# Performance work log

Hardware: AMD Instinct MI355X
Metric: run time of the kernel (lower is better)

## Reference

```python
import jax, jax.numpy as jnp
import numpy as np

B, C, K, H, W = 8, 64, 32, 128, 128  # K = num_cluster // 2
NEG_SLOPE = 0.1


def setup_inputs() -> dict:
    key = jax.random.key(0)
    k1, k2, k3, k4, k5, k6 = jax.random.split(key, 6)
    HR = jax.random.normal(k1, (B, C, H, W), jnp.float32)
    LR = jax.random.normal(k2, (B, C, H, W), jnp.float32)
    # Conv2d(1+K, 1, 1) weights flattened to [1+K] + bias, Conv2d(1,1,1) -> scalar w/b
    w1 = jax.random.normal(k3, (K + 1,), jnp.float32) * 0.1
    b1 = jax.random.normal(k4, (1,), jnp.float32) * 0.1
    w2 = jax.random.normal(k5, (1,), jnp.float32) * 0.1
    b2 = jax.random.normal(k6, (1,), jnp.float32) * 0.1
    return {"HR": HR, "LR": LR, "w1": w1, "b1": b1, "w2": w2, "b2": b2}


def reference(HR, LR, w1, b1, w2, b2):
    Bn, Cn = HR.shape[0], HR.shape[1]
    HRf = HR.reshape(Bn, Cn, -1)                      # [B, C, HW]
    LRf = LR.reshape(Bn, Cn, -1)                      # [B, C, HW]
    corr = jnp.einsum('bcn,bdn->bcd', LRf, HRf)       # [B, C_lr, C_hr]
    _, idx = jax.lax.top_k(corr, K)                   # [B, C, K] (int32)
    # gather top-K HR channels per LR channel: [B, C, K, H, W]
    gathered = jax.vmap(lambda h, ix: h[ix])(HR, idx)
    weight = jax.nn.sigmoid(jnp.max(gathered, axis=2))        # [B, C, H, W]
    # 1x1 conv over the (1+K) concatenated channels == weighted sum
    fusion = w1[0] * LR + jnp.einsum('bckhw,k->bchw', gathered, w1[1:]) + b1[0]
    fusion = jnp.where(fusion >= 0, fusion, NEG_SLOPE * fusion)  # LeakyReLU(0.1)
    fusion = w2[0] * fusion + b2[0]                   # second 1x1 conv
    return fusion * (1.0 + weight)                    # fusion + weight*fusion
```

## Files before the change

### kernel.cpp

```cpp
#include <hip/hip_runtime.h>
#include <math.h>

#define B_ 8
#define C_ 64
#define K_ 32
#define HW_ 16384
#define NCHUNKOUT_ 64
#define TILE_ 256
#define NEG_SLOPE_ 0.1f


__device__ __forceinline__ void gl_lds16(const float* g, float* l) {
    __builtin_amdgcn_global_load_lds(
        (const __attribute__((address_space(1))) void*)g,
        (__attribute__((address_space(3))) void*)l,
        16, 0, 0);
}

__global__ __launch_bounds__(256, 2) void corr_partial_kernel(
    const float* __restrict__ LR, const float* __restrict__ HR,
    float* __restrict__ partial)
{
    __shared__ float smem[16384];
    float* lrS = smem;
    float* hrS = smem + 8192;

    const int bid = blockIdx.x;
    const int b = bid >> 6;
    const int q = bid & 63;
    const int t = threadIdx.x;
    const int wv = t >> 6;
    const int lane = t & 63;
    const int cq = lane >> 3;
    const int dq = lane & 7;

    float acc[8][8] = {};

    #pragma unroll 1
    for (int it = 0; it < 2; ++it) {
        const int n0 = q * 256 + it * 128;
        if (it) __syncthreads();

        #pragma unroll
        for (int s = 0; s < 8; ++s) {
            const int r0 = wv * 16 + s * 2;
            const int row = r0 + (lane >> 5);
            const int cl = (((lane & 31) * 4) ^ ((row & 7) * 4));
            const size_t goff = (size_t)(b * C_ + row) * HW_ + n0 + cl;
            gl_lds16(&LR[goff], &lrS[r0 * 128]);
            gl_lds16(&HR[goff], &hrS[r0 * 128]);
        }
        __syncthreads();

        #pragma unroll
        for (int nq = 0; nq < 8; ++nq) {
            const int col = wv * 32 + nq * 4;
            const int cxl = col ^ (cq * 4);
            const int cxh = col ^ (dq * 4);
            float4 lv[8];
            #pragma unroll
            for (int i = 0; i < 8; ++i)
                lv[i] = *reinterpret_cast<const float4*>(&lrS[(cq + 8 * i) * 128 + cxl]);
            #pragma unroll
            for (int j = 0; j < 8; ++j) {
                const float4 hv = *reinterpret_cast<const float4*>(&hrS[(dq + 8 * j) * 128 + cxh]);
                #pragma unroll
                for (int i = 0; i < 8; ++i) {
                    acc[i][j] = fmaf(lv[i].x, hv.x, acc[i][j]);
                    acc[i][j] = fmaf(lv[i].y, hv.y, acc[i][j]);
                    acc[i][j] = fmaf(lv[i].z, hv.z, acc[i][j]);
                    acc[i][j] = fmaf(lv[i].w, hv.w, acc[i][j]);
                }
            }
        }
    }

    __syncthreads();
    float* red = smem;
    #pragma unroll
    for (int sl = 0; sl < 16; ++sl) {
        const int i = sl >> 1;
        const int j0 = (sl & 1) * 4;
        *reinterpret_cast<float4*>(&red[((wv * 16 + sl) * 64 + lane) * 4]) =
            make_float4(acc[i][j0], acc[i][j0 + 1], acc[i][j0 + 2], acc[i][j0 + 3]);
    }
    __syncthreads();

    float* P = partial + (size_t)bid * (C_ * C_);
    #pragma unroll
    for (int pp = 0; pp < 4; ++pp) {
        const int sl = wv * 4 + pp;
        float4 s = make_float4(0.f, 0.f, 0.f, 0.f);
        #pragma unroll
        for (int w = 0; w < 4; ++w) {
            const float4 v = *reinterpret_cast<const float4*>(
                &red[((w * 16 + sl) * 64 + lane) * 4]);
            s.x += v.x; s.y += v.y; s.z += v.z; s.w += v.w;
        }
        const int i = sl >> 1;
        const int j0 = (sl & 1) * 4;
        const int row = (lane >> 3) + 8 * i;
        const int colb = (lane & 7) + 8 * j0;
        P[row * C_ + colb]      = s.x;
        P[row * C_ + colb + 8]  = s.y;
        P[row * C_ + colb + 16] = s.z;
        P[row * C_ + colb + 24] = s.w;
    }
}

__global__ __launch_bounds__(64) void rank_kernel(
    const float* __restrict__ partial, int* __restrict__ idxb)
{
    __shared__ double vals[C_];
    const int blk = blockIdx.x;
    const int b = blk >> 6;
    const int c = blk & 63;
    const int d = threadIdx.x;

    double acc = 0.0;
    for (int k = 0; k < NCHUNKOUT_; ++k)
        acc += (double)partial[(size_t)(b * NCHUNKOUT_ + k) * (C_ * C_) + c * C_ + d];
    vals[d] = acc;
    __syncthreads();

    int r = 0;
    for (int jj = 0; jj < C_; ++jj) {
        const double vj = vals[jj];
        r += (int)((vj > acc) || (vj == acc && jj < d));
    }
    if (r < K_) idxb[blk * K_ + r] = d;
}

__global__ __launch_bounds__(512, 2) void fusion_gather_kernel(
    const float* __restrict__ HR, const float* __restrict__ LR,
    const int* __restrict__ idxb,
    const float* __restrict__ w1, const float* __restrict__ b1,
    const float* __restrict__ w2, const float* __restrict__ b2,
    float* __restrict__ out)
{
    __shared__ float hrS[C_][TILE_];

    const int t = threadIdx.x;
    const int bid = blockIdx.x;
    const int b = bid >> 6;
    const int px0 = (bid & 63) * TILE_;

    const float* HRb = HR + (size_t)b * C_ * HW_;
    #pragma unroll
    for (int i = 0; i < 8; ++i) {
        const int f = i * 512 + t;
        const int c = f >> 6;
        const int qq = f & 63;
        *reinterpret_cast<float4*>(&hrS[c][qq * 4]) =
            *reinterpret_cast<const float4*>(&HRb[(size_t)c * HW_ + px0 + qq * 4]);
    }
    __syncthreads();

    const int wv = t >> 6;
    const int lane = t & 63;
    const int p4 = lane * 4;

    const int* idxc = idxb + b * C_ * K_;
    const float w10 = w1[0];
    const float b1v = b1[0], w2v = w2[0], b2v = b2[0];

    #pragma unroll 1
    for (int ci = 0; ci < 8; ++ci) {
        const int c = wv * 8 + ci;
        const float4 l4 = *reinterpret_cast<const float4*>(
            &LR[(size_t)(b * C_ + c) * HW_ + px0 + p4]);
        float acc[4] = {0.f, 0.f, 0.f, 0.f};
        float mx[4]  = {-1e30f, -1e30f, -1e30f, -1e30f};
        #pragma unroll
        for (int k = 0; k < K_; ++k) {
            const int d = idxc[c * K_ + k];
            const float4 h = *reinterpret_cast<const float4*>(&hrS[d][p4]);
            const float wk = w1[k + 1];
            acc[0] = fmaf(h.x, wk, acc[0]);
            acc[1] = fmaf(h.y, wk, acc[1]);
            acc[2] = fmaf(h.z, wk, acc[2]);
            acc[3] = fmaf(h.w, wk, acc[3]);
            mx[0] = fmaxf(mx[0], h.x);
            mx[1] = fmaxf(mx[1], h.y);
            mx[2] = fmaxf(mx[2], h.z);
            mx[3] = fmaxf(mx[3], h.w);
        }
        const float l[4] = {l4.x, l4.y, l4.z, l4.w};
        float o[4];
        #pragma unroll
        for (int p = 0; p < 4; ++p) {
            float f = fmaf(w10, l[p], acc[p]) + b1v;
            f = f >= 0.f ? f : NEG_SLOPE_ * f;
            f = fmaf(w2v, f, b2v);
            const float s = 1.f / (1.f + __expf(-mx[p]));
            o[p] = f * (1.f + s);
        }
        *reinterpret_cast<float4*>(&out[(size_t)(b * C_ + c) * HW_ + px0 + p4]) =
            make_float4(o[0], o[1], o[2], o[3]);
    }
}

extern "C" void kernel_launch(void* const* d_in, const int* in_sizes, int n_in,
                              void* d_out, int out_size, void* d_ws, size_t ws_size,
                              hipStream_t stream)
{
    const float* HR = (const float*)d_in[0];
    const float* LR = (const float*)d_in[1];
    const float* w1 = (const float*)d_in[2];
    const float* b1 = (const float*)d_in[3];
    const float* w2 = (const float*)d_in[4];
    const float* b2 = (const float*)d_in[5];
    float* out = (float*)d_out;

    float* partial = (float*)d_ws;
    int* idxb = (int*)((char*)d_ws + (size_t)B_ * NCHUNKOUT_ * C_ * C_ * sizeof(float));

    corr_partial_kernel<<<B_ * 64, 256, 0, stream>>>(LR, HR, partial);
    rank_kernel<<<B_ * C_, 64, 0, stream>>>(partial, idxb);
    fusion_gather_kernel<<<B_ * (HW_ / TILE_), 512, 0, stream>>>(HR, LR, idxb, w1, b1, w2, b2, out);
}
```

Measured before the change: 73.53 us.

## Register-prefetch corr tiles with padded LDS and halve block count

Replaces the direct global-to-LDS async loads with register-staged float4 loads that prefetch the next 128-column chunk while the current chunk is computed. It switches the XOR swizzle to a padded LDS row stride of 132, and each block now covers 512 columns over four iterations instead of 256 over two. The partial-sum count per batch drops to 32, which halves the rank kernel's reduction reads. In exchange, register pressure rises from the 16 prefetch float4s, and only 256 blocks are launched, which may underfill the GPU.

```diff
diff --git a/kernel.cpp b/kernel.cpp
--- a/kernel.cpp
+++ b/kernel.cpp
@@ -5,65 +5,80 @@
 #define C_ 64
 #define K_ 32
 #define HW_ 16384
-#define NCHUNKOUT_ 64
+#define LDN 132
+#define NCHUNKOUT_ 32
 #define TILE_ 256
 #define NEG_SLOPE_ 0.1f
 
-
-__device__ __forceinline__ void gl_lds16(const float* g, float* l) {
-    __builtin_amdgcn_global_load_lds(
-        (const __attribute__((address_space(1))) void*)g,
-        (__attribute__((address_space(3))) void*)l,
-        16, 0, 0);
-}
 
 __global__ __launch_bounds__(256, 2) void corr_partial_kernel(
     const float* __restrict__ LR, const float* __restrict__ HR,
     float* __restrict__ partial)
 {
-    __shared__ float smem[16384];
+    __shared__ float smem[2 * C_ * LDN];
     float* lrS = smem;
-    float* hrS = smem + 8192;
+    float* hrS = smem + C_ * LDN;
 
     const int bid = blockIdx.x;
-    const int b = bid >> 6;
-    const int q = bid & 63;
+    const int b = bid >> 5;
+    const int q = bid & 31;
     const int t = threadIdx.x;
     const int wv = t >> 6;
     const int lane = t & 63;
     const int cq = lane >> 3;
     const int dq = lane & 7;
 
+    int sc[8], scol[8];
+    #pragma unroll
+    for (int p = 0; p < 8; ++p) {
+        const int f = p * 256 + t;
+        sc[p] = f >> 5;
+        scol[p] = (f & 31) * 4;
+    }
+
+    float4 sLR[8], sHR[8];
+    {
+        const int n0 = q * 512;
+        #pragma unroll
+        for (int p = 0; p < 8; ++p) {
+            const size_t g = (size_t)(b * C_ + sc[p]) * HW_ + n0 + scol[p];
+            sLR[p] = *reinterpret_cast<const float4*>(&LR[g]);
+            sHR[p] = *reinterpret_cast<const float4*>(&HR[g]);
+        }
+    }
+
     float acc[8][8] = {};
 
     #pragma unroll 1
-    for (int it = 0; it < 2; ++it) {
-        const int n0 = q * 256 + it * 128;
-        if (it) __syncthreads();
-
-        #pragma unroll
-        for (int s = 0; s < 8; ++s) {
-            const int r0 = wv * 16 + s * 2;
-            const int row = r0 + (lane >> 5);
-            const int cl = (((lane & 31) * 4) ^ ((row & 7) * 4));
-            const size_t goff = (size_t)(b * C_ + row) * HW_ + n0 + cl;
-            gl_lds16(&LR[goff], &lrS[r0 * 128]);
-            gl_lds16(&HR[goff], &hrS[r0 * 128]);
+    for (int ck = 0; ck < 4; ++ck) {
+        if (ck) __syncthreads();
+        #pragma unroll
+        for (int p = 0; p < 8; ++p) {
+            *reinterpret_cast<float4*>(&lrS[sc[p] * LDN + scol[p]]) = sLR[p];
+            *reinterpret_cast<float4*>(&hrS[sc[p] * LDN + scol[p]]) = sHR[p];
         }
         __syncthreads();
+
+        if (ck < 3) {
+            const int n0 = q * 512 + (ck + 1) * 128;
+            #pragma unroll
+            for (int p = 0; p < 8; ++p) {
+                const size_t g = (size_t)(b * C_ + sc[p]) * HW_ + n0 + scol[p];
+                sLR[p] = *reinterpret_cast<const float4*>(&LR[g]);
+                sHR[p] = *reinterpret_cast<const float4*>(&HR[g]);
+            }
+        }
 
         #pragma unroll
         for (int nq = 0; nq < 8; ++nq) {
             const int col = wv * 32 + nq * 4;
-            const int cxl = col ^ (cq * 4);
-            const int cxh = col ^ (dq * 4);
             float4 lv[8];
             #pragma unroll
             for (int i = 0; i < 8; ++i)
-                lv[i] = *reinterpret_cast<const float4*>(&lrS[(cq + 8 * i) * 128 + cxl]);
+                lv[i] = *reinterpret_cast<const float4*>(&lrS[(cq + 8 * i) * LDN + col]);
             #pragma unroll
             for (int j = 0; j < 8; ++j) {
-                const float4 hv = *reinterpret_cast<const float4*>(&hrS[(dq + 8 * j) * 128 + cxh]);
+                const float4 hv = *reinterpret_cast<const float4*>(&hrS[(dq + 8 * j) * LDN + col]);
                 #pragma unroll
                 for (int i = 0; i < 8; ++i) {
                     acc[i][j] = fmaf(lv[i].x, hv.x, acc[i][j]);
@@ -215,7 +230,7 @@
     float* partial = (float*)d_ws;
     int* idxb = (int*)((char*)d_ws + (size_t)B_ * NCHUNKOUT_ * C_ * C_ * sizeof(float));
 
-    corr_partial_kernel<<<B_ * 64, 256, 0, stream>>>(LR, HR, partial);
+    corr_partial_kernel<<<B_ * 32, 256, 0, stream>>>(LR, HR, partial);
     rank_kernel<<<B_ * C_, 64, 0, stream>>>(partial, idxb);
     fusion_gather_kernel<<<B_ * (HW_ / TILE_), 512, 0, stream>>>(HR, LR, idxb, w1, b1, w2, b2, out);
 }
```

After: 86.02 us. 1.17x slower.
